# Kernel optimization log

Hardware: AMD Instinct MI355X
Metric: run time of the kernel (lower is better)

The kernel has to match this reference:

```python
import jax, jax.numpy as jnp
import numpy as np
import math


def setup_inputs() -> dict:
    rng = jax.random.key(0)
    k1, k2, k3 = jax.random.split(rng, 3)
    B, L, H, E = 2, 1024, 8, 64
    query = jax.random.normal(k1, (B, L, H, E), dtype=jnp.float32)
    key = jax.random.normal(k2, (B, L, H, E), dtype=jnp.float32)
    value = jax.random.normal(k3, (B, L, H, E), dtype=jnp.float32)
    mask_miss_k = jnp.zeros((B, L), dtype=bool)
    mask_miss_q = jnp.zeros((B, L), dtype=bool)
    pos = jnp.arange(B * L).reshape(B, L)
    causal_mask = 0  # unused by the module body
    # learned scalar parameters (nn.Parameter init values)
    log_gain_gate = jnp.float32(math.log(2.0))
    log_tau_gate = jnp.float32(math.log(0.5))
    log_gain_dir = jnp.float32(math.log(3.0))
    log_tau_dir = jnp.float32(math.log(0.3))
    return {
        "query": query, "key": key, "value": value,
        "mask_miss_k": mask_miss_k, "mask_miss_q": mask_miss_q,
        "pos": pos, "causal_mask": causal_mask,
        "log_gain_gate": log_gain_gate, "log_tau_gate": log_tau_gate,
        "log_gain_dir": log_gain_dir, "log_tau_dir": log_tau_dir,
    }


def reference(query, key, value, mask_miss_k, mask_miss_q, pos, causal_mask,
              log_gain_gate, log_tau_gate, log_gain_dir, log_tau_dir):
    # Multihead path: query (B,L,H,E). Eval mode, dropout p=0, dag_mask=None.
    B, L, H, E = query.shape
    scale = 1.0 / jnp.sqrt(jnp.float32(E))
    # scores: (B,H,L,S) with S == L
    scores = scale * jnp.einsum('blhe,bshe->bhls', query, key)
    scores_t = jnp.swapaxes(scores, -1, -2)
    S_sym = 0.5 * (scores + scores_t)       # symmetric part
    A_anti = 0.5 * (scores - scores_t)      # antisymmetric (Lie) part

    MAX_GAIN = 20.0
    gain_gate = jnp.clip(jnp.exp(log_gain_gate), 1e-3, MAX_GAIN)
    tau_gate = jnp.clip(jnp.exp(log_tau_gate), 1e-3, 10.0)
    gain_dir = jnp.clip(jnp.exp(log_gain_dir), 1e-3, MAX_GAIN)
    tau_dir = jnp.clip(jnp.exp(log_tau_dir), 1e-3, 10.0)

    gamma_att = gain_gate * jnp.tanh(S_sym / tau_gate)
    phi_att = gain_dir * jnp.tanh(A_anti / tau_dir)

    gate_probs = jax.nn.sigmoid(gamma_att)
    dir_probs = jax.nn.sigmoid(phi_att)
    dag_probs = gate_probs * dir_probs

    diag = jnp.eye(L, L, dtype=bool)  # P(i->i) = 0
    dag_probs = jnp.where(diag[None, None], 0.0, dag_probs)
    M = dag_probs  # eval branch; diagonal already zeroed (second fill is a no-op)

    att = jax.nn.relu(jnp.tanh(A_anti * gain_dir / tau_dir)) * M

    # entropy per query position (B,H,L)
    entropy = -jnp.sum(att * jnp.log(jnp.clip(att, 1e-8, None)), axis=-1)
    entropy = jnp.nan_to_num(entropy)

    # dropout p=0 -> identity; nan_to_num is a no-op on finite att
    V = jnp.einsum('bhls,bshd->blhd', att, value)  # (B,L,H,E)
    return V, att, entropy
```

## Files before the change

### kernel.cpp

```cpp
#include <hip/hip_runtime.h>
#include <math.h>

namespace {

typedef __bf16 bf16_t;
typedef bf16_t bf16x8 __attribute__((ext_vector_type(8)));
typedef bf16_t bf16x4 __attribute__((ext_vector_type(4)));
typedef bf16_t bf16x2 __attribute__((ext_vector_type(2)));
typedef float f32x4 __attribute__((ext_vector_type(4)));

constexpr int L = 1024;
constexpr int H = 8;
constexpr int E = 64;
constexpr int HE = H * E;
constexpr int BH = 16;
constexpr size_t PL = (size_t)BH * L * E;

__device__ __forceinline__ float rcp_fast(float x) { return __builtin_amdgcn_rcpf(x); }
__device__ __forceinline__ float tanh_fast(float x) {
  return 1.0f - 2.0f * rcp_fast(__expf(2.0f * x) + 1.0f);
}
__device__ __forceinline__ float sigm_fast(float x) {
  return rcp_fast(1.0f + __expf(-x));
}
__device__ __forceinline__ f32x4 mfma16(bf16x8 a, bf16x8 b, f32x4 c) {
  return __builtin_amdgcn_mfma_f32_16x16x32_bf16(a, b, c, 0, 0, 0);
}
__device__ __forceinline__ void split4(float4 x, bf16x4& hv, bf16x4& lv) {
  hv[0] = (bf16_t)x.x; lv[0] = (bf16_t)(x.x - (float)hv[0]);
  hv[1] = (bf16_t)x.y; lv[1] = (bf16_t)(x.y - (float)hv[1]);
  hv[2] = (bf16_t)x.z; lv[2] = (bf16_t)(x.z - (float)hv[2]);
  hv[3] = (bf16_t)x.w; lv[3] = (bf16_t)(x.w - (float)hv[3]);
}

__global__ __launch_bounds__(256) void k_prep(
    const float* __restrict__ q, const float* __restrict__ k,
    const float* __restrict__ v, bf16_t* __restrict__ ws)
{
  bf16_t* Qh = ws;
  bf16_t* Ql = ws + PL;
  bf16_t* Kh = ws + 2 * PL;
  bf16_t* Kl = ws + 3 * PL;
  bf16_t* VT = ws + 4 * PL;
  const int bh = blockIdx.x >> 3, chunk = blockIdx.x & 7;
  const int b = bh >> 3, h = bh & 7;
  const int tid = threadIdx.x, t8 = tid >> 4, c4 = tid & 15;
  __shared__ bf16_t Vb[64][136];

#pragma unroll
  for (int pass = 0; pass < 8; ++pass) {
    const int row = chunk * 128 + pass * 16 + t8;
    const size_t gin = ((size_t)(b * L + row) * H + h) * E + c4 * 4;
    const size_t gout = ((size_t)bh * L + row) * E + c4 * 4;
    float4 q4 = *(const float4*)(q + gin);
    float4 k4 = *(const float4*)(k + gin);
    float4 v4 = *(const float4*)(v + gin);
    bf16x4 hv, lv;
    split4(q4, hv, lv);
    *(bf16x4*)(Qh + gout) = hv; *(bf16x4*)(Ql + gout) = lv;
    split4(k4, hv, lv);
    *(bf16x4*)(Kh + gout) = hv; *(bf16x4*)(Kl + gout) = lv;
    const int sl = pass * 16 + t8;
    Vb[c4 * 4 + 0][sl] = (bf16_t)v4.x;
    Vb[c4 * 4 + 1][sl] = (bf16_t)v4.y;
    Vb[c4 * 4 + 2][sl] = (bf16_t)v4.z;
    Vb[c4 * 4 + 3][sl] = (bf16_t)v4.w;
  }
  __syncthreads();
#pragma unroll
  for (int pass = 0; pass < 4; ++pass) {
    const int idx = pass * 256 + tid;
    const int e = idx >> 4, ch = idx & 15;
    bf16x8 val = *(const bf16x8*)&Vb[e][ch * 8];
    *(bf16x8*)(VT + ((size_t)bh * E + e) * L + chunk * 128 + ch * 8) = val;
  }
}

__global__ __launch_bounds__(256) void k_zero(float* __restrict__ Vout,
                                              float* __restrict__ entr)
{
  const int idx = blockIdx.x * 256 + threadIdx.x;
  const float4 z = make_float4(0.f, 0.f, 0.f, 0.f);
  if (idx < 262144) *(float4*)(Vout + (size_t)idx * 4) = z;
  else              *(float4*)(entr + (size_t)(idx - 262144) * 4) = z;
}

__global__ __launch_bounds__(256, 3) void k_main(
    const bf16_t* __restrict__ ws,
    float* __restrict__ Vout, float* __restrict__ attg, float* __restrict__ entr,
    const float* __restrict__ p_lgg, const float* __restrict__ p_ltg,
    const float* __restrict__ p_lgd, const float* __restrict__ p_ltd)
{
  const bf16_t* Qh = ws;
  const bf16_t* Ql = ws + PL;
  const bf16_t* Kh = ws + 2 * PL;
  const bf16_t* Kl = ws + 3 * PL;
  const bf16_t* VT = ws + 4 * PL;

  __shared__ __align__(16) char smem[32768];
  bf16_t (*KQh)[72]  = (bf16_t(*)[72])(smem);
  bf16_t (*KQl)[72]  = (bf16_t(*)[72])(smem + 9216);
  bf16_t (*Vt)[72]   = (bf16_t(*)[72])(smem + 18432);
  bf16_t (*attL)[40] = (bf16_t(*)[40])(smem + 27648);

  const int tid = threadIdx.x;
  const int w = tid >> 6, lane = tid & 63;
  const int c = lane & 15, qd = lane >> 4;
  const int lh = w & 1, sh = w >> 1;
  const int lt = blockIdx.x, bh = blockIdx.y, zb = blockIdx.z;
  const int b = bh >> 3, h = bh & 7;
  const int l0 = lt * 32;

  const float gg = fminf(fmaxf(__expf(p_lgg[0]), 1e-3f), 20.0f);
  const float tg = fminf(fmaxf(__expf(p_ltg[0]), 1e-3f), 10.0f);
  const float gd = fminf(fmaxf(__expf(p_lgd[0]), 1e-3f), 20.0f);
  const float td = fminf(fmaxf(__expf(p_ltd[0]), 1e-3f), 10.0f);
  const float inv_tg = 1.0f / tg;
  const float inv_td = 1.0f / td;
  const float gd_inv_td = gd * inv_td;

  bf16x8 qaf[2][2], kaf[2][2];
  {
    const size_t aro = ((size_t)bh * L + l0 + lh * 16 + c) * E;
#pragma unroll
    for (int ks = 0; ks < 2; ++ks) {
      qaf[ks][0] = *(const bf16x8*)(Qh + aro + ks * 32 + qd * 8);
      qaf[ks][1] = *(const bf16x8*)(Ql + aro + ks * 32 + qd * 8);
      kaf[ks][0] = *(const bf16x8*)(Kh + aro + ks * 32 + qd * 8);
      kaf[ks][1] = *(const bf16x8*)(Kl + aro + ks * 32 + qd * 8);
    }
  }

  const int srow = tid >> 2, scol = (tid & 3) * 16;

  bf16x8 kh8a, kh8b, kl8a, kl8b, vt8a, vt8b, qh8a, qh8b, ql8a, ql8b;
  {
    const int s0 = zb * 8 * 64;
    const size_t off = ((size_t)bh * L + s0 + srow) * E + scol;
    kh8a = *(const bf16x8*)(Kh + off);
    kh8b = *(const bf16x8*)(Kh + off + 8);
    kl8a = *(const bf16x8*)(Kl + off);
    kl8b = *(const bf16x8*)(Kl + off + 8);
    const size_t voff = ((size_t)bh * E + srow) * L + s0 + scol;
    vt8a = *(const bf16x8*)(VT + voff);
    vt8b = *(const bf16x8*)(VT + voff + 8);
  }

  f32x4 accv[4] = {};
  float ent[4] = {0.f, 0.f, 0.f, 0.f};

  for (int it = 0; it < 8; ++it) {
    const int ti = zb * 8 + it;
    const int s0 = ti * 64;
    const int s0n = ((ti + 1) & 15) * 64;

    __syncthreads();
    *(bf16x8*)&KQh[srow][scol]     = kh8a;
    *(bf16x8*)&KQh[srow][scol + 8] = kh8b;
    *(bf16x8*)&KQl[srow][scol]     = kl8a;
    *(bf16x8*)&KQl[srow][scol + 8] = kl8b;
    *(bf16x8*)&Vt[srow][scol]      = vt8a;
    *(bf16x8*)&Vt[srow][scol + 8]  = vt8b;
    {
      const size_t off = ((size_t)bh * L + s0 + srow) * E + scol;
      qh8a = *(const bf16x8*)(Qh + off);
      qh8b = *(const bf16x8*)(Qh + off + 8);
      ql8a = *(const bf16x8*)(Ql + off);
      ql8b = *(const bf16x8*)(Ql + off + 8);
    }
    __syncthreads();

    f32x4 acc1[2] = {}, acc2[2] = {};
#pragma unroll
    for (int nt = 0; nt < 2; ++nt) {
      const int brow = sh * 32 + nt * 16 + c;
#pragma unroll
      for (int ks = 0; ks < 2; ++ks) {
        bf16x8 bhv = *(const bf16x8*)&KQh[brow][ks * 32 + qd * 8];
        bf16x8 blv = *(const bf16x8*)&KQl[brow][ks * 32 + qd * 8];
        acc1[nt] = mfma16(qaf[ks][0], bhv, acc1[nt]);
        acc1[nt] = mfma16(qaf[ks][0], blv, acc1[nt]);
        acc1[nt] = mfma16(qaf[ks][1], bhv, acc1[nt]);
      }
    }
    __syncthreads();

    *(bf16x8*)&KQh[srow][scol]     = qh8a;
    *(bf16x8*)&KQh[srow][scol + 8] = qh8b;
    *(bf16x8*)&KQl[srow][scol]     = ql8a;
    *(bf16x8*)&KQl[srow][scol + 8] = ql8b;
    {
      const size_t off = ((size_t)bh * L + s0n + srow) * E + scol;
      kh8a = *(const bf16x8*)(Kh + off);
      kh8b = *(const bf16x8*)(Kh + off + 8);
      kl8a = *(const bf16x8*)(Kl + off);
      kl8b = *(const bf16x8*)(Kl + off + 8);
      const size_t voff = ((size_t)bh * E + srow) * L + s0n + scol;
      vt8a = *(const bf16x8*)(VT + voff);
      vt8b = *(const bf16x8*)(VT + voff + 8);
    }
    __syncthreads();

#pragma unroll
    for (int nt = 0; nt < 2; ++nt) {
      const int brow = sh * 32 + nt * 16 + c;
#pragma unroll
      for (int ks = 0; ks < 2; ++ks) {
        bf16x8 qbh = *(const bf16x8*)&KQh[brow][ks * 32 + qd * 8];
        bf16x8 qbl = *(const bf16x8*)&KQl[brow][ks * 32 + qd * 8];
        acc2[nt] = mfma16(kaf[ks][0], qbh, acc2[nt]);
        acc2[nt] = mfma16(kaf[ks][1], qbh, acc2[nt]);
        acc2[nt] = mfma16(kaf[ks][0], qbl, acc2[nt]);
      }
    }

    float* arow = attg + ((size_t)bh * L + l0 + lh * 16 + qd * 4) * L + s0 + sh * 32;
#pragma unroll
    for (int nt = 0; nt < 2; ++nt) {
#pragma unroll
      for (int r = 0; r < 4; ++r) {
        float x = 0.125f * acc1[nt][r];
        float y = 0.125f * acc2[nt][r];
        float Ss = 0.5f * (x + y);
        float Aa = 0.5f * (x - y);
        float gate = sigm_fast(gg * tanh_fast(Ss * inv_tg));
        float dir  = sigm_fast(gd * tanh_fast(Aa * inv_td));
        float t    = tanh_fast(Aa * gd_inv_td);
        float a = fmaxf(t, 0.0f) * gate * dir;
        ent[r] -= a * __logf(fmaxf(a, 1e-8f));
        arow[(size_t)r * L + nt * 16 + c] = a;
        attL[w * 16 + qd * 4 + r][nt * 16 + c] = (bf16_t)a;
      }
    }
    __threadfence_block();

    bf16x8 af = *(const bf16x8*)&attL[w * 16 + c][qd * 8];
#pragma unroll
    for (int ne = 0; ne < 4; ++ne) {
      bf16x8 bv = *(const bf16x8*)&Vt[ne * 16 + c][sh * 32 + qd * 8];
      accv[ne] = mfma16(af, bv, accv[ne]);
    }
  }

  __syncthreads();
  float* red = (float*)smem;
  if (sh == 1) {
#pragma unroll
    for (int ne = 0; ne < 4; ++ne)
#pragma unroll
      for (int r = 0; r < 4; ++r)
        red[((size_t)lh * 16 + qd * 4 + r) * 68 + ne * 16 + c] = accv[ne][r];
  }
  __syncthreads();
  if (sh == 0) {
#pragma unroll
    for (int ne = 0; ne < 4; ++ne)
#pragma unroll
      for (int r = 0; r < 4; ++r) {
        float val = accv[ne][r] +
                    red[((size_t)lh * 16 + qd * 4 + r) * 68 + ne * 16 + c];
        atomicAdd(Vout + ((size_t)(b * L + l0 + lh * 16 + qd * 4 + r) * H + h) * E +
                      ne * 16 + c,
                  val);
      }
  }
#pragma unroll
  for (int r = 0; r < 4; ++r) {
    float e = ent[r];
    e += __shfl_xor(e, 1);
    e += __shfl_xor(e, 2);
    e += __shfl_xor(e, 4);
    e += __shfl_xor(e, 8);
    if (c == 0)
      atomicAdd(entr + (size_t)bh * L + l0 + lh * 16 + qd * 4 + r, e);
  }
}

__device__ __forceinline__ void split_store(bf16_t* hi, bf16_t* lo, float4 x) {
  bf16x4 hv, lv;
  split4(x, hv, lv);
  *(bf16x4*)hi = hv;
  *(bf16x4*)lo = lv;
}

__global__ __launch_bounds__(128, 1) void fused_attn(
    const float* __restrict__ q, const float* __restrict__ kk,
    const float* __restrict__ v,
    float* __restrict__ Vout, float* __restrict__ attg, float* __restrict__ entr,
    const float* __restrict__ p_lgg, const float* __restrict__ p_ltg,
    const float* __restrict__ p_lgd, const float* __restrict__ p_ltd)
{
  constexpr int TM = 32;
  __shared__ bf16_t Qa_hi[TM][72], Qa_lo[TM][72];
  __shared__ bf16_t Ka_hi[TM][72], Ka_lo[TM][72];
  __shared__ bf16_t KQ_hi[64][72], KQ_lo[64][72];
  __shared__ bf16_t Vts[64][72];
  __shared__ float  T2ex[2][64][17];
  __shared__ bf16_t attLs[2][16][72];

  const int tid = threadIdx.x;
  const int w = tid >> 6;
  const int lane = tid & 63;
  const int c = lane & 15;
  const int qd = lane >> 4;
  const int t8 = tid >> 4;
  const int c4 = tid & 15;
  const int lt = blockIdx.x;
  const int bh = blockIdx.y;
  const int b = bh >> 3, h = bh & 7;
  const int l0 = lt * TM;

  const float gg = fminf(fmaxf(__expf(p_lgg[0]), 1e-3f), 20.0f);
  const float tg = fminf(fmaxf(__expf(p_ltg[0]), 1e-3f), 10.0f);
  const float gd = fminf(fmaxf(__expf(p_lgd[0]), 1e-3f), 20.0f);
  const float td = fminf(fmaxf(__expf(p_ltd[0]), 1e-3f), 10.0f);
  const float inv_tg = 1.0f / tg;
  const float inv_td = 1.0f / td;
  const float gd_inv_td = gd * inv_td;

  const float* qlbase = q  + ((size_t)(b * L + l0) * H + h) * E;
  const float* qsbase = q  + ((size_t)b * L * H + h) * E;
  const float* kbase  = kk + ((size_t)b * L * H + h) * E;
  const float* vbase  = v  + ((size_t)b * L * H + h) * E;

#pragma unroll
  for (int i = 0; i < 4; ++i) {
    int r = t8 + 8 * i;
    float4 qa = *(const float4*)(qlbase + (size_t)r * HE + c4 * 4);
    float4 ka = *(const float4*)(kbase + (size_t)(l0 + r) * HE + c4 * 4);
    split_store(&Qa_hi[r][c4 * 4], &Qa_lo[r][c4 * 4], qa);
    split_store(&Ka_hi[r][c4 * 4], &Ka_lo[r][c4 * 4], ka);
  }

  float4 kpre[8], qpre[8];
  float vpre[32];
#pragma unroll
  for (int i = 0; i < 8; ++i)
    kpre[i] = *(const float4*)(kbase + (size_t)(t8 + 8 * i) * HE + c4 * 4);
#pragma unroll
  for (int i = 0; i < 8; ++i)
    qpre[i] = *(const float4*)(qsbase + (size_t)(t8 + 8 * i) * HE + c4 * 4);
#pragma unroll
  for (int j = 0; j < 32; ++j)
    vpre[j] = vbase[(size_t)(w * 32 + j) * HE + lane];

  __syncthreads();

  bf16x8 qaf[2][2], kaf[2][2];
#pragma unroll
  for (int ks = 0; ks < 2; ++ks) {
    qaf[ks][0] = *(const bf16x8*)&Qa_hi[w * 16 + c][ks * 32 + qd * 8];
    qaf[ks][1] = *(const bf16x8*)&Qa_lo[w * 16 + c][ks * 32 + qd * 8];
    kaf[ks][0] = *(const bf16x8*)&Ka_hi[w * 16 + c][ks * 32 + qd * 8];
    kaf[ks][1] = *(const bf16x8*)&Ka_lo[w * 16 + c][ks * 32 + qd * 8];
  }

  f32x4 accv[4] = {};
  float ent[4] = {0.f, 0.f, 0.f, 0.f};
  const int gl_base = l0 + w * 16 + qd * 4;

  for (int it = 0; it < 16; ++it) {
    const int s0 = it * 64;
    const int snext = ((it + 1) & 15) * 64;

    __syncthreads();
#pragma unroll
    for (int i = 0; i < 8; ++i) {
      int r = t8 + 8 * i;
      split_store(&KQ_hi[r][c4 * 4], &KQ_lo[r][c4 * 4], kpre[i]);
    }
#pragma unroll
    for (int j = 0; j < 16; ++j) {
      bf16x2 p;
      p[0] = (bf16_t)vpre[2 * j];
      p[1] = (bf16_t)vpre[2 * j + 1];
      *(bf16x2*)&Vts[lane][w * 32 + 2 * j] = p;
    }
    __syncthreads();

#pragma unroll
    for (int i = 0; i < 8; ++i)
      kpre[i] = *(const float4*)(kbase + (size_t)(snext + t8 + 8 * i) * HE + c4 * 4);
#pragma unroll
    for (int j = 0; j < 32; ++j)
      vpre[j] = vbase[(size_t)(snext + w * 32 + j) * HE + lane];

    f32x4 acc1[4] = {};
#pragma unroll
    for (int nt = 0; nt < 4; ++nt) {
#pragma unroll
      for (int ks = 0; ks < 2; ++ks) {
        bf16x8 bhv = *(const bf16x8*)&KQ_hi[nt * 16 + c][ks * 32 + qd * 8];
        bf16x8 blv = *(const bf16x8*)&KQ_lo[nt * 16 + c][ks * 32 + qd * 8];
        acc1[nt] = mfma16(qaf[ks][0], bhv, acc1[nt]);
        acc1[nt] = mfma16(qaf[ks][0], blv, acc1[nt]);
        acc1[nt] = mfma16(qaf[ks][1], bhv, acc1[nt]);
      }
    }
    __syncthreads();

#pragma unroll
    for (int i = 0; i < 8; ++i) {
      int r = t8 + 8 * i;
      split_store(&KQ_hi[r][c4 * 4], &KQ_lo[r][c4 * 4], qpre[i]);
    }
    __syncthreads();

#pragma unroll
    for (int i = 0; i < 8; ++i)
      qpre[i] = *(const float4*)(qsbase + (size_t)(snext + t8 + 8 * i) * HE + c4 * 4);

    f32x4 acc2[4] = {};
#pragma unroll
    for (int mt = 0; mt < 4; ++mt) {
#pragma unroll
      for (int ks = 0; ks < 2; ++ks) {
        bf16x8 ahv = *(const bf16x8*)&KQ_hi[mt * 16 + c][ks * 32 + qd * 8];
        bf16x8 alv = *(const bf16x8*)&KQ_lo[mt * 16 + c][ks * 32 + qd * 8];
        acc2[mt] = mfma16(ahv, kaf[ks][0], acc2[mt]);
        acc2[mt] = mfma16(ahv, kaf[ks][1], acc2[mt]);
        acc2[mt] = mfma16(alv, kaf[ks][0], acc2[mt]);
      }
    }

#pragma unroll
    for (int mt = 0; mt < 4; ++mt)
#pragma unroll
      for (int r = 0; r < 4; ++r)
        T2ex[w][mt * 16 + qd * 4 + r][c] = acc2[mt][r];
    __syncthreads();

    float* attrow0 = attg + ((size_t)bh * L + gl_base) * L + s0;
#pragma unroll
    for (int nt = 0; nt < 4; ++nt) {
#pragma unroll
      for (int r = 0; r < 4; ++r) {
        float x = 0.125f * acc1[nt][r];
        float y = 0.125f * T2ex[w][nt * 16 + c][qd * 4 + r];
        float Ss = 0.5f * (x + y);
        float Aa = 0.5f * (x - y);
        float gate = sigm_fast(gg * tanh_fast(Ss * inv_tg));
        float dir  = sigm_fast(gd * tanh_fast(Aa * inv_td));
        float t    = tanh_fast(Aa * gd_inv_td);
        float a = fmaxf(t, 0.0f) * gate * dir;
        ent[r] -= a * __logf(fmaxf(a, 1e-8f));
        attrow0[(size_t)r * L + nt * 16 + c] = a;
        attLs[w][qd * 4 + r][nt * 16 + c] = (bf16_t)a;
      }
    }
    __syncthreads();

#pragma unroll
    for (int ks = 0; ks < 2; ++ks) {
      bf16x8 af = *(const bf16x8*)&attLs[w][c][ks * 32 + qd * 8];
#pragma unroll
      for (int ne = 0; ne < 4; ++ne) {
        bf16x8 bfv = *(const bf16x8*)&Vts[ne * 16 + c][ks * 32 + qd * 8];
        accv[ne] = mfma16(af, bfv, accv[ne]);
      }
    }
  }

#pragma unroll
  for (int r = 0; r < 4; ++r) {
    float* vb = Vout + ((size_t)(b * L + gl_base + r) * H + h) * E;
#pragma unroll
    for (int ne = 0; ne < 4; ++ne) vb[ne * 16 + c] = accv[ne][r];
    float e4 = ent[r];
    e4 += __shfl_xor(e4, 1);
    e4 += __shfl_xor(e4, 2);
    e4 += __shfl_xor(e4, 4);
    e4 += __shfl_xor(e4, 8);
    if (c == 0) entr[(size_t)bh * L + gl_base + r] = e4;
  }
}

}

extern "C" void kernel_launch(void* const* d_in, const int* in_sizes, int n_in,
                              void* d_out, int out_size, void* d_ws, size_t ws_size,
                              hipStream_t stream) {
  const float* q = (const float*)d_in[0];
  const float* k = (const float*)d_in[1];
  const float* v = (const float*)d_in[2];
  const float* p_lgg = (const float*)d_in[7];
  const float* p_ltg = (const float*)d_in[8];
  const float* p_lgd = (const float*)d_in[9];
  const float* p_ltd = (const float*)d_in[10];

  float* Vout = (float*)d_out;
  float* att  = Vout + 1048576;
  float* entr = att + 16777216;

  const size_t need = 5 * PL * sizeof(bf16_t);
  if (ws_size >= need) {
    bf16_t* ws = (bf16_t*)d_ws;
    k_prep<<<dim3(128), 256, 0, stream>>>(q, k, v, ws);
    k_zero<<<dim3(1040), 256, 0, stream>>>(Vout, entr);
    k_main<<<dim3(32, 16, 2), 256, 0, stream>>>(
        ws, Vout, att, entr, p_lgg, p_ltg, p_lgd, p_ltd);
  } else {
    fused_attn<<<dim3(32, 16), 128, 0, stream>>>(
        q, k, v, Vout, att, entr, p_lgg, p_ltg, p_lgd, p_ltd);
  }
}
```

Baseline: 150.8 us.

## Merge zeroing into prep, split key range four ways, use exp2/log2 math

The zeroing kernel is folded into the prep kernel as extra blocks, removing one launch. Prep now uses 256 smaller chunks instead of 128. The main kernel's key dimension is split into four z-slices instead of two, doubling the block count at the cost of more atomic adds on the outputs. The elementwise gating math is rewritten to fold scales and log2e into constants and use native exp2/log2 instructions, with the entropy rescaled by ln2 at the end.

```diff
diff --git a/kernel.cpp b/kernel.cpp
--- a/kernel.cpp
+++ b/kernel.cpp
@@ -15,14 +15,12 @@
 constexpr int HE = H * E;
 constexpr int BH = 16;
 constexpr size_t PL = (size_t)BH * L * E;
+constexpr float LOG2E = 1.4426950408889634f;
+constexpr float LN2 = 0.6931471805599453f;
 
 __device__ __forceinline__ float rcp_fast(float x) { return __builtin_amdgcn_rcpf(x); }
-__device__ __forceinline__ float tanh_fast(float x) {
-  return 1.0f - 2.0f * rcp_fast(__expf(2.0f * x) + 1.0f);
-}
-__device__ __forceinline__ float sigm_fast(float x) {
-  return rcp_fast(1.0f + __expf(-x));
-}
+__device__ __forceinline__ float exp2_fast(float x) { return __builtin_amdgcn_exp2f(x); }
+__device__ __forceinline__ float log2_fast(float x) { return __builtin_amdgcn_logf(x); }
 __device__ __forceinline__ f32x4 mfma16(bf16x8 a, bf16x8 b, f32x4 c) {
   return __builtin_amdgcn_mfma_f32_16x16x32_bf16(a, b, c, 0, 0, 0);
 }
@@ -35,21 +33,30 @@
 
 __global__ __launch_bounds__(256) void k_prep(
     const float* __restrict__ q, const float* __restrict__ k,
-    const float* __restrict__ v, bf16_t* __restrict__ ws)
+    const float* __restrict__ v, bf16_t* __restrict__ ws,
+    float* __restrict__ Vout, float* __restrict__ entr)
 {
+  const int bid = blockIdx.x;
+  if (bid >= 256) {
+    const int idx = (bid - 256) * 256 + threadIdx.x;
+    const float4 z = make_float4(0.f, 0.f, 0.f, 0.f);
+    if (idx < 262144) *(float4*)(Vout + (size_t)idx * 4) = z;
+    else              *(float4*)(entr + (size_t)(idx - 262144) * 4) = z;
+    return;
+  }
   bf16_t* Qh = ws;
   bf16_t* Ql = ws + PL;
   bf16_t* Kh = ws + 2 * PL;
   bf16_t* Kl = ws + 3 * PL;
   bf16_t* VT = ws + 4 * PL;
-  const int bh = blockIdx.x >> 3, chunk = blockIdx.x & 7;
+  const int bh = bid >> 4, chunk = bid & 15;
   const int b = bh >> 3, h = bh & 7;
   const int tid = threadIdx.x, t8 = tid >> 4, c4 = tid & 15;
-  __shared__ bf16_t Vb[64][136];
-
-#pragma unroll
-  for (int pass = 0; pass < 8; ++pass) {
-    const int row = chunk * 128 + pass * 16 + t8;
+  __shared__ bf16_t Vb[64][72];
+
+#pragma unroll
+  for (int pass = 0; pass < 4; ++pass) {
+    const int row = chunk * 64 + pass * 16 + t8;
     const size_t gin = ((size_t)(b * L + row) * H + h) * E + c4 * 4;
     const size_t gout = ((size_t)bh * L + row) * E + c4 * 4;
     float4 q4 = *(const float4*)(q + gin);
@@ -68,21 +75,12 @@
   }
   __syncthreads();
 #pragma unroll
-  for (int pass = 0; pass < 4; ++pass) {
+  for (int pass = 0; pass < 2; ++pass) {
     const int idx = pass * 256 + tid;
-    const int e = idx >> 4, ch = idx & 15;
+    const int e = idx >> 3, ch = idx & 7;
     bf16x8 val = *(const bf16x8*)&Vb[e][ch * 8];
-    *(bf16x8*)(VT + ((size_t)bh * E + e) * L + chunk * 128 + ch * 8) = val;
-  }
-}
-
-__global__ __launch_bounds__(256) void k_zero(float* __restrict__ Vout,
-                                              float* __restrict__ entr)
-{
-  const int idx = blockIdx.x * 256 + threadIdx.x;
-  const float4 z = make_float4(0.f, 0.f, 0.f, 0.f);
-  if (idx < 262144) *(float4*)(Vout + (size_t)idx * 4) = z;
-  else              *(float4*)(entr + (size_t)(idx - 262144) * 4) = z;
+    *(bf16x8*)(VT + ((size_t)bh * E + e) * L + chunk * 64 + ch * 8) = val;
+  }
 }
 
 __global__ __launch_bounds__(256, 3) void k_main(
@@ -115,9 +113,11 @@
   const float tg = fminf(fmaxf(__expf(p_ltg[0]), 1e-3f), 10.0f);
   const float gd = fminf(fmaxf(__expf(p_lgd[0]), 1e-3f), 20.0f);
   const float td = fminf(fmaxf(__expf(p_ltd[0]), 1e-3f), 10.0f);
-  const float inv_tg = 1.0f / tg;
-  const float inv_td = 1.0f / td;
-  const float gd_inv_td = gd * inv_td;
+  const float A1 = 0.125f * (1.0f / tg) * LOG2E;
+  const float A2 = 0.125f * (1.0f / td) * LOG2E;
+  const float A3 = 0.125f * gd * (1.0f / td) * LOG2E;
+  const float G1 = -gg * LOG2E;
+  const float G2 = -gd * LOG2E;
 
   bf16x8 qaf[2][2], kaf[2][2];
   {
@@ -135,7 +135,7 @@
 
   bf16x8 kh8a, kh8b, kl8a, kl8b, vt8a, vt8b, qh8a, qh8b, ql8a, ql8b;
   {
-    const int s0 = zb * 8 * 64;
+    const int s0 = zb * 4 * 64;
     const size_t off = ((size_t)bh * L + s0 + srow) * E + scol;
     kh8a = *(const bf16x8*)(Kh + off);
     kh8b = *(const bf16x8*)(Kh + off + 8);
@@ -149,8 +149,8 @@
   f32x4 accv[4] = {};
   float ent[4] = {0.f, 0.f, 0.f, 0.f};
 
-  for (int it = 0; it < 8; ++it) {
-    const int ti = zb * 8 + it;
+  for (int it = 0; it < 4; ++it) {
+    const int ti = zb * 4 + it;
     const int s0 = ti * 64;
     const int s0n = ((ti + 1) & 15) * 64;
 
@@ -219,15 +219,15 @@
     for (int nt = 0; nt < 2; ++nt) {
 #pragma unroll
       for (int r = 0; r < 4; ++r) {
-        float x = 0.125f * acc1[nt][r];
-        float y = 0.125f * acc2[nt][r];
-        float Ss = 0.5f * (x + y);
-        float Aa = 0.5f * (x - y);
-        float gate = sigm_fast(gg * tanh_fast(Ss * inv_tg));
-        float dir  = sigm_fast(gd * tanh_fast(Aa * inv_td));
-        float t    = tanh_fast(Aa * gd_inv_td);
+        float u = acc1[nt][r] + acc2[nt][r];
+        float d = acc1[nt][r] - acc2[nt][r];
+        float th1 = 1.f - 2.f * rcp_fast(exp2_fast(u * A1) + 1.f);
+        float gate = rcp_fast(1.f + exp2_fast(th1 * G1));
+        float th2 = 1.f - 2.f * rcp_fast(exp2_fast(d * A2) + 1.f);
+        float dir  = rcp_fast(1.f + exp2_fast(th2 * G2));
+        float t    = 1.f - 2.f * rcp_fast(exp2_fast(d * A3) + 1.f);
         float a = fmaxf(t, 0.0f) * gate * dir;
-        ent[r] -= a * __logf(fmaxf(a, 1e-8f));
+        ent[r] -= a * log2_fast(fmaxf(a, 1e-8f));
         arow[(size_t)r * L + nt * 16 + c] = a;
         attL[w * 16 + qd * 4 + r][nt * 16 + c] = (bf16_t)a;
       }
@@ -272,10 +272,16 @@
     e += __shfl_xor(e, 4);
     e += __shfl_xor(e, 8);
     if (c == 0)
-      atomicAdd(entr + (size_t)bh * L + l0 + lh * 16 + qd * 4 + r, e);
-  }
-}
-
+      atomicAdd(entr + (size_t)bh * L + l0 + lh * 16 + qd * 4 + r, e * LN2);
+  }
+}
+
+__device__ __forceinline__ float tanh_fast(float x) {
+  return 1.0f - 2.0f * rcp_fast(__expf(2.0f * x) + 1.0f);
+}
+__device__ __forceinline__ float sigm_fast(float x) {
+  return rcp_fast(1.0f + __expf(-x));
+}
 __device__ __forceinline__ void split_store(bf16_t* hi, bf16_t* lo, float4 x) {
   bf16x4 hv, lv;
   split4(x, hv, lv);
@@ -495,9 +501,8 @@
   const size_t need = 5 * PL * sizeof(bf16_t);
   if (ws_size >= need) {
     bf16_t* ws = (bf16_t*)d_ws;
-    k_prep<<<dim3(128), 256, 0, stream>>>(q, k, v, ws);
-    k_zero<<<dim3(1040), 256, 0, stream>>>(Vout, entr);
-    k_main<<<dim3(32, 16, 2), 256, 0, stream>>>(
+    k_prep<<<dim3(1296), 256, 0, stream>>>(q, k, v, ws, Vout, entr);
+    k_main<<<dim3(32, 16, 4), 256, 0, stream>>>(
         ws, Vout, att, entr, p_lgg, p_ltg, p_lgd, p_ltd);
   } else {
     fused_attn<<<dim3(32, 16), 128, 0, stream>>>(
```

Measured after the change: 137.8 us. 1.09x faster.
